# Optimization experiments

Measured on AMD Instinct MI355X. Metric: run time of the kernel, lower is better.

Reference implementation:

```python
import jax, jax.numpy as jnp
import numpy as np

HIDDEN = 4096
W = 16          # wave_units
LN_EPS = 1e-5   # torch LayerNorm default


def _layernorm(x, gamma, beta):
    mu = jnp.mean(x, axis=-1, keepdims=True)
    var = jnp.mean(jnp.square(x - mu), axis=-1, keepdims=True)
    return (x - mu) * jax.lax.rsqrt(var + LN_EPS) * gamma + beta


def setup_inputs() -> dict:
    key = jax.random.key(0)
    ks = jax.random.split(key, 12)
    B, S, H = 4, 4096, HIDDEN
    hidden_states = jax.random.normal(ks[0], (B, S, H), dtype=jnp.float32)
    frequencies = jax.random.uniform(ks[1], (W,), dtype=jnp.float32) * 2.0
    phases = jax.random.uniform(ks[2], (W,), dtype=jnp.float32) * (2 * np.pi)
    coupling_raw = jax.random.normal(ks[3], (W, W), dtype=jnp.float32) * 0.1
    mask = jax.random.uniform(ks[4], (W, W)) < 0.75  # coupling_density
    coupling = coupling_raw * mask.astype(jnp.float32)
    damping = jnp.ones((W,), dtype=jnp.float32) * 0.1
    # input_proj: Linear(H, 2W) -> LN -> SiLU -> Linear(2W, W)
    w1 = jax.random.normal(ks[5], (H, 2 * W), dtype=jnp.float32) * 0.02
    b1 = jnp.zeros((2 * W,), dtype=jnp.float32)
    g1 = jnp.ones((2 * W,), dtype=jnp.float32)
    beta1 = jnp.zeros((2 * W,), dtype=jnp.float32)
    w2 = jax.random.normal(ks[6], (2 * W, W), dtype=jnp.float32) * 0.02
    b2 = jnp.zeros((W,), dtype=jnp.float32)
    # output_proj: Linear(W, 2W) -> LN -> SiLU -> Linear(2W, H)
    w3 = jax.random.normal(ks[7], (W, 2 * W), dtype=jnp.float32) * 0.02
    b3 = jnp.zeros((2 * W,), dtype=jnp.float32)
    g2 = jnp.ones((2 * W,), dtype=jnp.float32)
    beta2 = jnp.zeros((2 * W,), dtype=jnp.float32)
    w4 = jax.random.normal(ks[8], (2 * W, H), dtype=jnp.float32) * 0.02
    b4 = jnp.zeros((H,), dtype=jnp.float32)
    time_step = jnp.float32(0.0)  # buffer; incremented by 0.1 each call
    return dict(hidden_states=hidden_states, frequencies=frequencies, phases=phases,
                coupling=coupling, damping=damping,
                w1=w1, b1=b1, g1=g1, beta1=beta1, w2=w2, b2=b2,
                w3=w3, b3=b3, g2=g2, beta2=beta2, w4=w4, b4=b4,
                time_step=time_step)


def reference(hidden_states, frequencies, phases, coupling, damping,
              w1, b1, g1, beta1, w2, b2,
              w3, b3, g2, beta2, w4, b4, time_step):
    x = hidden_states.astype(jnp.float32)  # [B,S,H]
    t = time_step + 0.1
    # input_proj: [B,S,H] -> [B,S,W]
    h = jnp.einsum('bsh,hd->bsd', x, w1) + b1
    h = jax.nn.silu(_layernorm(h, g1, beta1))
    wave_input = jnp.einsum('bsd,dw->bsw', h, w2) + b2
    # base waves are identical for every (b, s): compute once on [W]
    base_waves = jnp.sin(2 * np.pi * frequencies * t + phases) * jnp.exp(-damping * t)
    coupled = jnp.tanh(base_waves @ coupling)  # [W]
    modulated = coupled * (1.0 + wave_input)   # [B,S,W]
    mean_waves = jnp.mean(modulated, axis=(0, 1))  # [W]
    # buffers start at zero: resonance = 0.9*0 + 0.1*|mean_waves|
    resonance = 0.1 * jnp.abs(mean_waves)
    resonance_factor = jax.nn.sigmoid(jnp.mean(resonance))
    # output_proj: [B,S,W] -> [B,S,H]
    o = jnp.einsum('bsw,wd->bsd', modulated, w3) + b3
    o = jax.nn.silu(_layernorm(o, g2, beta2))
    wave_output = jnp.einsum('bsd,dh->bsh', o, w4) + b4
    return hidden_states + wave_output * resonance_factor
```

## Files before the change

kernel.cpp:

```cpp
#include <hip/hip_runtime.h>
#include <hip/hip_bf16.h>
#include <math.h>

#define HID 4096
#define R_TOTAL 16384

typedef __attribute__((ext_vector_type(8))) short short8;
typedef __attribute__((ext_vector_type(8))) unsigned short ushort8;
typedef __attribute__((ext_vector_type(4))) float f32x4;

__device__ __forceinline__ ushort bfc(float f) {
  __hip_bfloat16 h = __float2bfloat16(f);
  return *(ushort*)&h;
}

__global__ __launch_bounds__(256) void wn_prep(
    const float* __restrict__ w1, const float* __restrict__ w4,
    ushort* __restrict__ w1T, ushort* __restrict__ w4T,
    const float* __restrict__ freq, const float* __restrict__ phases,
    const float* __restrict__ coupling, const float* __restrict__ damping,
    const float* __restrict__ tstep, float* __restrict__ cpl)
{
  __shared__ ushort tile[64*72];
  __shared__ float base[16];
  const int b = blockIdx.x, t = threadIdx.x;
  if (b < 64) {
    #pragma unroll
    for (int i = 0; i < 8; ++i) {
      const int e = t + i*256, kk = e >> 5, c = e & 31;
      tile[c*72 + kk] = bfc(w1[(size_t)(b*64+kk)*32 + c]);
    }
    __syncthreads();
    const int c = t >> 3, j = t & 7;
    ushort8 v;
    #pragma unroll
    for (int q = 0; q < 8; ++q) v[q] = tile[c*72 + j*8 + q];
    *(ushort8*)&w1T[(size_t)c*HID + b*64 + j*8] = v;
  } else if (b < 128) {
    const int b2 = b - 64;
    #pragma unroll
    for (int i = 0; i < 8; ++i) {
      const int e = t + i*256, d = e >> 6, hh = e & 63;
      tile[hh*40 + d] = bfc(w4[(size_t)d*HID + b2*64 + hh]);
    }
    __syncthreads();
    const int hh = t >> 2, j = t & 3;
    ushort8 v;
    #pragma unroll
    for (int q = 0; q < 8; ++q) v[q] = tile[hh*40 + j*8 + q];
    *(ushort8*)&w4T[(size_t)(b2*64+hh)*32 + j*8] = v;
  } else {
    const float tt = tstep[0] + 0.1f;
    if (t < 16)
      base[t] = sinf(6.283185307179586f*freq[t]*tt + phases[t]) * expf(-damping[t]*tt);
    __syncthreads();
    if (t < 16) {
      float s = 0.f;
      #pragma unroll
      for (int i = 0; i < 16; ++i) s += base[i]*coupling[i*16+t];
      cpl[t] = tanhf(s);
    }
  }
}

__global__ __launch_bounds__(256) void wn_phase1(
    const float* __restrict__ x, const ushort* __restrict__ w1T,
    const float* __restrict__ b1, const float* __restrict__ g1,
    const float* __restrict__ beta1, const float* __restrict__ w2,
    const float* __restrict__ b2, const float* __restrict__ w3,
    const float* __restrict__ b3, const float* __restrict__ g2,
    const float* __restrict__ beta2, const float* __restrict__ cpl,
    ushort* __restrict__ o_ws, float* __restrict__ gacc)
{
  __shared__ __align__(16) float lds[10816];
  float* xbuf = lds;
  float* red  = lds;
  float* yl   = lds + 8192;
  float* w2l  = lds + 9248;
  float* w3l  = lds + 9760;
  float* msum = lds + 10272;
  const int t  = threadIdx.x;
  const int r0 = blockIdx.x * 32;

  if (t < 128) *(float4*)&w2l[t*4] = *(const float4*)&w2[t*4];
  else { const int u2 = t-128; *(float4*)&w3l[u2*4] = *(const float4*)&w3[u2*4]; }

  const int w    = t >> 6;
  const int l    = t & 63;
  const int mt   = w & 1, kh = w >> 1;
  const int lrow = l & 15, lkb = l >> 4;
  const int arow = mt*16 + lrow;
  const int aswz = arow & 7;

  f32x4 acc0 = {0.f,0.f,0.f,0.f}, acc1 = {0.f,0.f,0.f,0.f};
  float4 rg0, rg1, rg2, rg3;
  const int e0 = t, e1 = t+256, e2 = t+512, e3 = t+768;
  const int sr0 = e0>>5, su0 = e0&31, sr1 = e1>>5, su1 = e1&31;
  const int sr2 = e2>>5, su2 = e2&31, sr3 = e3>>5, su3 = e3&31;
  const int so0 = sr0*128 + (su0 ^ (sr0&7))*4;
  const int so1 = sr1*128 + (su1 ^ (sr1&7))*4;
  const int so2 = sr2*128 + (su2 ^ (sr2&7))*4;
  const int so3 = sr3*128 + (su3 ^ (sr3&7))*4;

  rg0 = *(const float4*)&x[(size_t)(r0+sr0)*HID + su0*4];
  rg1 = *(const float4*)&x[(size_t)(r0+sr1)*HID + su1*4];
  rg2 = *(const float4*)&x[(size_t)(r0+sr2)*HID + su2*4];
  rg3 = *(const float4*)&x[(size_t)(r0+sr3)*HID + su3*4];
  *(float4*)&xbuf[so0] = rg0;
  *(float4*)&xbuf[so1] = rg1;
  *(float4*)&xbuf[so2] = rg2;
  *(float4*)&xbuf[so3] = rg3;

  for (int it = 0; it < 32; ++it) {
    const int cur = it & 1;
    if (it < 31) {
      const int kc = (it+1)*128;
      rg0 = *(const float4*)&x[(size_t)(r0+sr0)*HID + kc + su0*4];
      rg1 = *(const float4*)&x[(size_t)(r0+sr1)*HID + kc + su1*4];
      rg2 = *(const float4*)&x[(size_t)(r0+sr2)*HID + kc + su2*4];
      rg3 = *(const float4*)&x[(size_t)(r0+sr3)*HID + kc + su3*4];
    }
    __syncthreads();
    const float* xb = &xbuf[cur*4096];
    #pragma unroll
    for (int s = 0; s < 2; ++s) {
      const int k0 = kh*64 + s*32;
      const int ub = (k0 >> 2) + lkb*2;
      const float4 a0 = *(const float4*)&xb[arow*128 + ((ub   ^ aswz))*4];
      const float4 a1 = *(const float4*)&xb[arow*128 + (((ub+1) ^ aswz))*4];
      short8 av;
      av[0] = (short)bfc(a0.x); av[1] = (short)bfc(a0.y);
      av[2] = (short)bfc(a0.z); av[3] = (short)bfc(a0.w);
      av[4] = (short)bfc(a1.x); av[5] = (short)bfc(a1.y);
      av[6] = (short)bfc(a1.z); av[7] = (short)bfc(a1.w);
      const int kg = it*128 + k0 + lkb*8;
      const short8 bv0 = *(const short8*)&w1T[(size_t)lrow*HID + kg];
      const short8 bv1 = *(const short8*)&w1T[(size_t)(16+lrow)*HID + kg];
      acc0 = __builtin_amdgcn_mfma_f32_16x16x32_bf16(av, bv0, acc0, 0, 0, 0);
      acc1 = __builtin_amdgcn_mfma_f32_16x16x32_bf16(av, bv1, acc1, 0, 0, 0);
    }
    __syncthreads();
    if (it < 31) {
      float* xn = &xbuf[(cur^1)*4096];
      *(float4*)&xn[so0] = rg0;
      *(float4*)&xn[so1] = rg1;
      *(float4*)&xn[so2] = rg2;
      *(float4*)&xn[so3] = rg3;
    }
  }
  __syncthreads();
  #pragma unroll
  for (int j = 0; j < 4; ++j) {
    red[kh*1056 + (mt*16 + lkb*4 + j)*33 + lrow]      = acc0[j];
    red[kh*1056 + (mt*16 + lkb*4 + j)*33 + 16 + lrow] = acc1[j];
  }
  __syncthreads();
  #pragma unroll
  for (int i = 0; i < 4; ++i) {
    const int e = t + i*256, row = e >> 5, col = e & 31;
    yl[row*33+col] = red[row*33+col] + red[1056 + row*33+col];
  }
  __syncthreads();
  if (t < 128) {
    const int row = t >> 2, q = t & 3, d0 = q*8;
    float v[8]; float mu = 0.f;
    #pragma unroll
    for (int dd = 0; dd < 8; ++dd) { v[dd] = yl[row*33 + d0+dd] + b1[d0+dd]; mu += v[dd]; }
    mu += __shfl_xor(mu,1); mu += __shfl_xor(mu,2); mu *= (1.f/32.f);
    float var = 0.f;
    #pragma unroll
    for (int dd = 0; dd < 8; ++dd) { const float c = v[dd]-mu; var += c*c; }
    var += __shfl_xor(var,1); var += __shfl_xor(var,2);
    const float rs = rsqrtf(var*(1.f/32.f) + 1e-5f);
    float wiv[16];
    #pragma unroll
    for (int ww = 0; ww < 16; ++ww) wiv[ww] = 0.f;
    #pragma unroll
    for (int dd = 0; dd < 8; ++dd) {
      const float hn = (v[dd]-mu)*rs*g1[d0+dd] + beta1[d0+dd];
      const float sl = hn / (1.f + __expf(-hn));
      const float* wr = &w2l[(d0+dd)*16];
      #pragma unroll
      for (int ww = 0; ww < 16; ++ww) wiv[ww] = fmaf(sl, wr[ww], wiv[ww]);
    }
    #pragma unroll
    for (int ww = 0; ww < 16; ++ww) {
      wiv[ww] += __shfl_xor(wiv[ww],1);
      wiv[ww] += __shfl_xor(wiv[ww],2);
    }
    float mod[16];
    #pragma unroll
    for (int ww = 0; ww < 16; ++ww) mod[ww] = cpl[ww]*(1.f + wiv[ww] + b2[ww]);
    #pragma unroll
    for (int j = 0; j < 4; ++j) msum[row*17 + q*4+j] = mod[q*4+j];
    float p[8];
    #pragma unroll
    for (int dd = 0; dd < 8; ++dd) p[dd] = b3[d0+dd];
    #pragma unroll
    for (int ww = 0; ww < 16; ++ww) {
      const float m = mod[ww];
      const float* wr = &w3l[ww*32 + d0];
      #pragma unroll
      for (int dd = 0; dd < 8; ++dd) p[dd] = fmaf(m, wr[dd], p[dd]);
    }
    float mu2 = 0.f;
    #pragma unroll
    for (int dd = 0; dd < 8; ++dd) mu2 += p[dd];
    mu2 += __shfl_xor(mu2,1); mu2 += __shfl_xor(mu2,2); mu2 *= (1.f/32.f);
    float var2 = 0.f;
    #pragma unroll
    for (int dd = 0; dd < 8; ++dd) { const float c = p[dd]-mu2; var2 += c*c; }
    var2 += __shfl_xor(var2,1); var2 += __shfl_xor(var2,2);
    const float rs2 = rsqrtf(var2*(1.f/32.f) + 1e-5f);
    ushort8 ov;
    #pragma unroll
    for (int dd = 0; dd < 8; ++dd) {
      const float hn = (p[dd]-mu2)*rs2*g2[d0+dd] + beta2[d0+dd];
      ov[dd] = bfc(hn / (1.f + __expf(-hn)));
    }
    *(ushort8*)&o_ws[(size_t)(r0+row)*32 + d0] = ov;
  }
  __syncthreads();
  if (t < 16) {
    float s = 0.f;
    for (int r = 0; r < 32; ++r) s += msum[r*17 + t];
    atomicAdd(gacc + t, s);
  }
}

__global__ void wn_phase2(const float* __restrict__ gacc, float* __restrict__ cpl)
{
  __shared__ float res[16];
  const int t = threadIdx.x;
  if (t < 16) res[t] = 0.1f * fabsf(gacc[t] * (1.f/(float)R_TOTAL));
  __syncthreads();
  if (t == 0) {
    float s = 0.f;
    #pragma unroll
    for (int ww = 0; ww < 16; ++ww) s += res[ww];
    cpl[16] = 1.f / (1.f + expf(-s*(1.f/16.f)));
  }
}

__global__ __launch_bounds__(256) void wn_phase3(
    const float* __restrict__ x, const ushort* __restrict__ o_bf,
    const ushort* __restrict__ w4T, const float* __restrict__ b4,
    const float* __restrict__ cpl, float* __restrict__ out)
{
  const int t = threadIdx.x, l = t & 63, w = t >> 6;
  const int bid = blockIdx.x;
  const int strip = bid & 7, m0 = (bid >> 3) * 64 + w*16;
  const float rf = cpl[16];
  const int lm = l & 15, lkb = l >> 4;
  const short8 bv = *(const short8*)&o_bf[(size_t)(m0+lm)*32 + lkb*8];
  const int mrow = m0 + lm;
  const size_t rowbase = (size_t)mrow*HID + strip*512 + lkb*4;
  #pragma unroll 2
  for (int nt = 0; nt < 32; ++nt) {
    const int n0 = strip*512 + nt*16;
    const short8 av = *(const short8*)&w4T[(size_t)(n0+lm)*32 + lkb*8];
    f32x4 c = {0.f,0.f,0.f,0.f};
    c = __builtin_amdgcn_mfma_f32_16x16x32_bf16(av, bv, c, 0, 0, 0);
    const size_t off = rowbase + (size_t)nt*16;
    const float4 xv  = *(const float4*)&x[off];
    const float4 b4v = *(const float4*)&b4[n0 + lkb*4];
    float4 o2;
    o2.x = fmaf(rf, c[0] + b4v.x, xv.x);
    o2.y = fmaf(rf, c[1] + b4v.y, xv.y);
    o2.z = fmaf(rf, c[2] + b4v.z, xv.z);
    o2.w = fmaf(rf, c[3] + b4v.w, xv.w);
    *(float4*)&out[off] = o2;
  }
}

extern "C" void kernel_launch(void* const* d_in, const int* in_sizes, int n_in,
                              void* d_out, int out_size, void* d_ws, size_t ws_size,
                              hipStream_t stream) {
  const float* x        = (const float*)d_in[0];
  const float* freq     = (const float*)d_in[1];
  const float* phases   = (const float*)d_in[2];
  const float* coupling = (const float*)d_in[3];
  const float* damping  = (const float*)d_in[4];
  const float* w1       = (const float*)d_in[5];
  const float* b1       = (const float*)d_in[6];
  const float* g1       = (const float*)d_in[7];
  const float* beta1    = (const float*)d_in[8];
  const float* w2       = (const float*)d_in[9];
  const float* b2       = (const float*)d_in[10];
  const float* w3       = (const float*)d_in[11];
  const float* b3       = (const float*)d_in[12];
  const float* g2       = (const float*)d_in[13];
  const float* beta2    = (const float*)d_in[14];
  const float* w4       = (const float*)d_in[15];
  const float* b4       = (const float*)d_in[16];
  const float* tstep    = (const float*)d_in[17];
  float* out = (float*)d_out;

  char* wsb = (char*)d_ws;
  ushort* o_bf = (ushort*)wsb;
  ushort* w1T  = (ushort*)(wsb + (1<<20));
  ushort* w4T  = (ushort*)(wsb + (1<<20) + (256<<10));
  float*  gacc = (float*)(wsb + (1<<20) + (512<<10));
  float*  cpl  = gacc + 16;

  hipMemsetAsync(gacc, 0, 16*sizeof(float), stream);
  hipLaunchKernelGGL(wn_prep, dim3(129), dim3(256), 0, stream,
                     w1, w4, w1T, w4T, freq, phases, coupling, damping, tstep, cpl);
  hipLaunchKernelGGL(wn_phase1, dim3(512), dim3(256), 0, stream,
                     x, w1T, b1, g1, beta1, w2, b2, w3, b3, g2, beta2, cpl, o_bf, gacc);
  hipLaunchKernelGGL(wn_phase2, dim3(1), dim3(64), 0, stream, gacc, cpl);
  hipLaunchKernelGGL(wn_phase3, dim3(2048), dim3(256), 0, stream,
                     x, o_bf, w4T, b4, cpl, out);
}
```

Measured before the change: 204.7 us.

## Load x directly into MFMA registers in phase1, split K across eight waves

```diff
diff --git a/kernel.cpp b/kernel.cpp
--- a/kernel.cpp
+++ b/kernel.cpp
@@ -63,7 +63,7 @@
   }
 }
 
-__global__ __launch_bounds__(256) void wn_phase1(
+__global__ __launch_bounds__(512, 4) void wn_phase1(
     const float* __restrict__ x, const ushort* __restrict__ w1T,
     const float* __restrict__ b1, const float* __restrict__ g1,
     const float* __restrict__ beta1, const float* __restrict__ w2,
@@ -72,100 +72,77 @@
     const float* __restrict__ beta2, const float* __restrict__ cpl,
     ushort* __restrict__ o_ws, float* __restrict__ gacc)
 {
-  __shared__ __align__(16) float lds[10816];
-  float* xbuf = lds;
+  __shared__ __align__(16) float lds[6720];
   float* red  = lds;
-  float* yl   = lds + 8192;
-  float* w2l  = lds + 9248;
-  float* w3l  = lds + 9760;
-  float* msum = lds + 10272;
+  float* yl   = lds + 4096;
+  float* w2l  = lds + 5152;
+  float* w3l  = lds + 5664;
+  float* msum = lds + 6176;
   const int t  = threadIdx.x;
   const int r0 = blockIdx.x * 32;
 
   if (t < 128) *(float4*)&w2l[t*4] = *(const float4*)&w2[t*4];
-  else { const int u2 = t-128; *(float4*)&w3l[u2*4] = *(const float4*)&w3[u2*4]; }
-
-  const int w    = t >> 6;
-  const int l    = t & 63;
-  const int mt   = w & 1, kh = w >> 1;
-  const int lrow = l & 15, lkb = l >> 4;
-  const int arow = mt*16 + lrow;
-  const int aswz = arow & 7;
+  else if (t < 256) { const int u2 = t-128; *(float4*)&w3l[u2*4] = *(const float4*)&w3[u2*4]; }
+
+  const int w  = t >> 6, l = t & 63;
+  const int mt = w & 1, kh = w >> 1;
+  const int lr = l & 15, lk = l >> 4;
+  const int row = r0 + mt*16 + lr;
+  const size_t xbase = (size_t)row*HID + kh*1024 + lk*8;
+  const ushort* bp0 = &w1T[(size_t)lr*HID + kh*1024 + lk*8];
+  const ushort* bp1 = bp0 + 16*HID;
 
   f32x4 acc0 = {0.f,0.f,0.f,0.f}, acc1 = {0.f,0.f,0.f,0.f};
-  float4 rg0, rg1, rg2, rg3;
-  const int e0 = t, e1 = t+256, e2 = t+512, e3 = t+768;
-  const int sr0 = e0>>5, su0 = e0&31, sr1 = e1>>5, su1 = e1&31;
-  const int sr2 = e2>>5, su2 = e2&31, sr3 = e3>>5, su3 = e3&31;
-  const int so0 = sr0*128 + (su0 ^ (sr0&7))*4;
-  const int so1 = sr1*128 + (su1 ^ (sr1&7))*4;
-  const int so2 = sr2*128 + (su2 ^ (sr2&7))*4;
-  const int so3 = sr3*128 + (su3 ^ (sr3&7))*4;
-
-  rg0 = *(const float4*)&x[(size_t)(r0+sr0)*HID + su0*4];
-  rg1 = *(const float4*)&x[(size_t)(r0+sr1)*HID + su1*4];
-  rg2 = *(const float4*)&x[(size_t)(r0+sr2)*HID + su2*4];
-  rg3 = *(const float4*)&x[(size_t)(r0+sr3)*HID + su3*4];
-  *(float4*)&xbuf[so0] = rg0;
-  *(float4*)&xbuf[so1] = rg1;
-  *(float4*)&xbuf[so2] = rg2;
-  *(float4*)&xbuf[so3] = rg3;
+  float4 a0 = *(const float4*)&x[xbase];
+  float4 a1 = *(const float4*)&x[xbase + 4];
+  short8 b0 = *(const short8*)bp0;
+  short8 b1v = *(const short8*)bp1;
 
   for (int it = 0; it < 32; ++it) {
-    const int cur = it & 1;
+    float4 na0, na1; short8 nb0, nb1;
     if (it < 31) {
-      const int kc = (it+1)*128;
-      rg0 = *(const float4*)&x[(size_t)(r0+sr0)*HID + kc + su0*4];
-      rg1 = *(const float4*)&x[(size_t)(r0+sr1)*HID + kc + su1*4];
-      rg2 = *(const float4*)&x[(size_t)(r0+sr2)*HID + kc + su2*4];
-      rg3 = *(const float4*)&x[(size_t)(r0+sr3)*HID + kc + su3*4];
-    }
-    __syncthreads();
-    const float* xb = &xbuf[cur*4096];
-    #pragma unroll
-    for (int s = 0; s < 2; ++s) {
-      const int k0 = kh*64 + s*32;
-      const int ub = (k0 >> 2) + lkb*2;
-      const float4 a0 = *(const float4*)&xb[arow*128 + ((ub   ^ aswz))*4];
-      const float4 a1 = *(const float4*)&xb[arow*128 + (((ub+1) ^ aswz))*4];
-      short8 av;
-      av[0] = (short)bfc(a0.x); av[1] = (short)bfc(a0.y);
-      av[2] = (short)bfc(a0.z); av[3] = (short)bfc(a0.w);
-      av[4] = (short)bfc(a1.x); av[5] = (short)bfc(a1.y);
-      av[6] = (short)bfc(a1.z); av[7] = (short)bfc(a1.w);
-      const int kg = it*128 + k0 + lkb*8;
-      const short8 bv0 = *(const short8*)&w1T[(size_t)lrow*HID + kg];
-      const short8 bv1 = *(const short8*)&w1T[(size_t)(16+lrow)*HID + kg];
-      acc0 = __builtin_amdgcn_mfma_f32_16x16x32_bf16(av, bv0, acc0, 0, 0, 0);
-      acc1 = __builtin_amdgcn_mfma_f32_16x16x32_bf16(av, bv1, acc1, 0, 0, 0);
-    }
-    __syncthreads();
-    if (it < 31) {
-      float* xn = &xbuf[(cur^1)*4096];
-      *(float4*)&xn[so0] = rg0;
-      *(float4*)&xn[so1] = rg1;
-      *(float4*)&xn[so2] = rg2;
-      *(float4*)&xn[so3] = rg3;
-    }
-  }
-  __syncthreads();
-  #pragma unroll
-  for (int j = 0; j < 4; ++j) {
-    red[kh*1056 + (mt*16 + lkb*4 + j)*33 + lrow]      = acc0[j];
-    red[kh*1056 + (mt*16 + lkb*4 + j)*33 + 16 + lrow] = acc1[j];
-  }
-  __syncthreads();
-  #pragma unroll
-  for (int i = 0; i < 4; ++i) {
-    const int e = t + i*256, row = e >> 5, col = e & 31;
-    yl[row*33+col] = red[row*33+col] + red[1056 + row*33+col];
+      const int ko = (it+1)*32;
+      na0 = *(const float4*)&x[xbase + ko];
+      na1 = *(const float4*)&x[xbase + ko + 4];
+      nb0 = *(const short8*)(bp0 + ko);
+      nb1 = *(const short8*)(bp1 + ko);
+    }
+    short8 av;
+    av[0] = (short)bfc(a0.x); av[1] = (short)bfc(a0.y);
+    av[2] = (short)bfc(a0.z); av[3] = (short)bfc(a0.w);
+    av[4] = (short)bfc(a1.x); av[5] = (short)bfc(a1.y);
+    av[6] = (short)bfc(a1.z); av[7] = (short)bfc(a1.w);
+    acc0 = __builtin_amdgcn_mfma_f32_16x16x32_bf16(av, b0, acc0, 0, 0, 0);
+    acc1 = __builtin_amdgcn_mfma_f32_16x16x32_bf16(av, b1v, acc1, 0, 0, 0);
+    a0 = na0; a1 = na1; b0 = nb0; b1v = nb1;
+  }
+  {
+    float* rp = &red[w*512 + l];
+    #pragma unroll
+    for (int j = 0; j < 4; ++j) { rp[j*64] = acc0[j]; rp[(4+j)*64] = acc1[j]; }
   }
   __syncthreads();
   if (t < 128) {
-    const int row = t >> 2, q = t & 3, d0 = q*8;
+    const int m2 = t >> 6, l2 = t & 63;
+    const int rr = m2*16 + (l2 >> 4)*4, cc = l2 & 15;
+    #pragma unroll
+    for (int j = 0; j < 4; ++j) {
+      float s0 = 0.f, s1 = 0.f;
+      #pragma unroll
+      for (int k = 0; k < 4; ++k) {
+        s0 += red[(m2 + 2*k)*512 + j*64 + l2];
+        s1 += red[(m2 + 2*k)*512 + (4+j)*64 + l2];
+      }
+      yl[(rr+j)*33 + cc]      = s0;
+      yl[(rr+j)*33 + 16 + cc] = s1;
+    }
+  }
+  __syncthreads();
+  if (t < 128) {
+    const int row2 = t >> 2, q = t & 3, d0 = q*8;
     float v[8]; float mu = 0.f;
     #pragma unroll
-    for (int dd = 0; dd < 8; ++dd) { v[dd] = yl[row*33 + d0+dd] + b1[d0+dd]; mu += v[dd]; }
+    for (int dd = 0; dd < 8; ++dd) { v[dd] = yl[row2*33 + d0+dd] + b1[d0+dd]; mu += v[dd]; }
     mu += __shfl_xor(mu,1); mu += __shfl_xor(mu,2); mu *= (1.f/32.f);
     float var = 0.f;
     #pragma unroll
@@ -192,7 +169,7 @@
     #pragma unroll
     for (int ww = 0; ww < 16; ++ww) mod[ww] = cpl[ww]*(1.f + wiv[ww] + b2[ww]);
     #pragma unroll
-    for (int j = 0; j < 4; ++j) msum[row*17 + q*4+j] = mod[q*4+j];
+    for (int j = 0; j < 4; ++j) msum[row2*17 + q*4+j] = mod[q*4+j];
     float p[8];
     #pragma unroll
     for (int dd = 0; dd < 8; ++dd) p[dd] = b3[d0+dd];
@@ -218,7 +195,7 @@
       const float hn = (p[dd]-mu2)*rs2*g2[d0+dd] + beta2[d0+dd];
       ov[dd] = bfc(hn / (1.f + __expf(-hn)));
     }
-    *(ushort8*)&o_ws[(size_t)(r0+row)*32 + d0] = ov;
+    *(ushort8*)&o_ws[(size_t)(r0+row2)*32 + d0] = ov;
   }
   __syncthreads();
   if (t < 16) {
@@ -255,7 +232,7 @@
   const short8 bv = *(const short8*)&o_bf[(size_t)(m0+lm)*32 + lkb*8];
   const int mrow = m0 + lm;
   const size_t rowbase = (size_t)mrow*HID + strip*512 + lkb*4;
-  #pragma unroll 2
+  #pragma unroll 4
   for (int nt = 0; nt < 32; ++nt) {
     const int n0 = strip*512 + nt*16;
     const short8 av = *(const short8*)&w4T[(size_t)(n0+lm)*32 + lkb*8];
@@ -306,7 +283,7 @@
   hipMemsetAsync(gacc, 0, 16*sizeof(float), stream);
   hipLaunchKernelGGL(wn_prep, dim3(129), dim3(256), 0, stream,
                      w1, w4, w1T, w4T, freq, phases, coupling, damping, tstep, cpl);
-  hipLaunchKernelGGL(wn_phase1, dim3(512), dim3(256), 0, stream,
+  hipLaunchKernelGGL(wn_phase1, dim3(512), dim3(512), 0, stream,
                      x, w1T, b1, g1, beta1, w2, b2, w3, b3, g2, beta2, cpl, o_bf, gacc);
   hipLaunchKernelGGL(wn_phase2, dim3(1), dim3(64), 0, stream, gacc, cpl);
   hipLaunchKernelGGL(wn_phase3, dim3(2048), dim3(256), 0, stream,
```

New measurement: 255.4 us. 24.7% more time.

## Stage x tile as bf16 in LDS, reverse phase3 row order, nontemporal output stores

Applied to the files above, without the earlier changes.

```diff
diff --git a/kernel.cpp b/kernel.cpp
--- a/kernel.cpp
+++ b/kernel.cpp
@@ -72,80 +72,85 @@
     const float* __restrict__ beta2, const float* __restrict__ cpl,
     ushort* __restrict__ o_ws, float* __restrict__ gacc)
 {
-  __shared__ __align__(16) float lds[10816];
-  float* xbuf = lds;
+  __shared__ __align__(16) float lds[6720];
+  ushort* xb  = (ushort*)lds;
   float* red  = lds;
-  float* yl   = lds + 8192;
-  float* w2l  = lds + 9248;
-  float* w3l  = lds + 9760;
-  float* msum = lds + 10272;
+  float* yl   = lds + 4096;
+  float* w2l  = lds + 5152;
+  float* w3l  = lds + 5664;
+  float* msum = lds + 6176;
   const int t  = threadIdx.x;
   const int r0 = blockIdx.x * 32;
 
   if (t < 128) *(float4*)&w2l[t*4] = *(const float4*)&w2[t*4];
   else { const int u2 = t-128; *(float4*)&w3l[u2*4] = *(const float4*)&w3[u2*4]; }
 
-  const int w    = t >> 6;
-  const int l    = t & 63;
+  const int srow = t >> 3, sc = t & 7;
+  const int wg0   = ((sc*2) ^ ((srow&7)<<1));
+  const int wbase = srow*128 + wg0*8;
+  const float* xp = &x[(size_t)(r0+srow)*HID + sc*16];
+
+  const int w    = t >> 6, l = t & 63;
   const int mt   = w & 1, kh = w >> 1;
   const int lrow = l & 15, lkb = l >> 4;
   const int arow = mt*16 + lrow;
-  const int aswz = arow & 7;
+  const int rsw  = (arow&7) << 1;
+  const int ra_s0 = arow*128 + ((kh*8 +     lkb) ^ rsw)*8;
+  const int ra_s1 = arow*128 + ((kh*8 + 4 + lkb) ^ rsw)*8;
+  const ushort* bp0 = &w1T[(size_t)lrow*HID + kh*64 + lkb*8];
+  const ushort* bp1 = bp0 + 16*HID;
 
   f32x4 acc0 = {0.f,0.f,0.f,0.f}, acc1 = {0.f,0.f,0.f,0.f};
   float4 rg0, rg1, rg2, rg3;
-  const int e0 = t, e1 = t+256, e2 = t+512, e3 = t+768;
-  const int sr0 = e0>>5, su0 = e0&31, sr1 = e1>>5, su1 = e1&31;
-  const int sr2 = e2>>5, su2 = e2&31, sr3 = e3>>5, su3 = e3&31;
-  const int so0 = sr0*128 + (su0 ^ (sr0&7))*4;
-  const int so1 = sr1*128 + (su1 ^ (sr1&7))*4;
-  const int so2 = sr2*128 + (su2 ^ (sr2&7))*4;
-  const int so3 = sr3*128 + (su3 ^ (sr3&7))*4;
-
-  rg0 = *(const float4*)&x[(size_t)(r0+sr0)*HID + su0*4];
-  rg1 = *(const float4*)&x[(size_t)(r0+sr1)*HID + su1*4];
-  rg2 = *(const float4*)&x[(size_t)(r0+sr2)*HID + su2*4];
-  rg3 = *(const float4*)&x[(size_t)(r0+sr3)*HID + su3*4];
-  *(float4*)&xbuf[so0] = rg0;
-  *(float4*)&xbuf[so1] = rg1;
-  *(float4*)&xbuf[so2] = rg2;
-  *(float4*)&xbuf[so3] = rg3;
+
+  rg0 = *(const float4*)&xp[0];
+  rg1 = *(const float4*)&xp[4];
+  rg2 = *(const float4*)&xp[8];
+  rg3 = *(const float4*)&xp[12];
+  {
+    ushort8 v0, v1;
+    v0[0]=bfc(rg0.x); v0[1]=bfc(rg0.y); v0[2]=bfc(rg0.z); v0[3]=bfc(rg0.w);
+    v0[4]=bfc(rg1.x); v0[5]=bfc(rg1.y); v0[6]=bfc(rg1.z); v0[7]=bfc(rg1.w);
+    v1[0]=bfc(rg2.x); v1[1]=bfc(rg2.y); v1[2]=bfc(rg2.z); v1[3]=bfc(rg2.w);
+    v1[4]=bfc(rg3.x); v1[5]=bfc(rg3.y); v1[6]=bfc(rg3.z); v1[7]=bfc(rg3.w);
+    *(ushort8*)&xb[wbase]     = v0;
+    *(ushort8*)&xb[wbase + 8] = v1;
+  }
 
   for (int it = 0; it < 32; ++it) {
     const int cur = it & 1;
     if (it < 31) {
       const int kc = (it+1)*128;
-      rg0 = *(const float4*)&x[(size_t)(r0+sr0)*HID + kc + su0*4];
-      rg1 = *(const float4*)&x[(size_t)(r0+sr1)*HID + kc + su1*4];
-      rg2 = *(const float4*)&x[(size_t)(r0+sr2)*HID + kc + su2*4];
-      rg3 = *(const float4*)&x[(size_t)(r0+sr3)*HID + kc + su3*4];
-    }
-    __syncthreads();
-    const float* xb = &xbuf[cur*4096];
-    #pragma unroll
-    for (int s = 0; s < 2; ++s) {
-      const int k0 = kh*64 + s*32;
-      const int ub = (k0 >> 2) + lkb*2;
-      const float4 a0 = *(const float4*)&xb[arow*128 + ((ub   ^ aswz))*4];
-      const float4 a1 = *(const float4*)&xb[arow*128 + (((ub+1) ^ aswz))*4];
-      short8 av;
-      av[0] = (short)bfc(a0.x); av[1] = (short)bfc(a0.y);
-      av[2] = (short)bfc(a0.z); av[3] = (short)bfc(a0.w);
-      av[4] = (short)bfc(a1.x); av[5] = (short)bfc(a1.y);
-      av[6] = (short)bfc(a1.z); av[7] = (short)bfc(a1.w);
-      const int kg = it*128 + k0 + lkb*8;
-      const short8 bv0 = *(const short8*)&w1T[(size_t)lrow*HID + kg];
-      const short8 bv1 = *(const short8*)&w1T[(size_t)(16+lrow)*HID + kg];
-      acc0 = __builtin_amdgcn_mfma_f32_16x16x32_bf16(av, bv0, acc0, 0, 0, 0);
-      acc1 = __builtin_amdgcn_mfma_f32_16x16x32_bf16(av, bv1, acc1, 0, 0, 0);
+      rg0 = *(const float4*)&xp[kc];
+      rg1 = *(const float4*)&xp[kc + 4];
+      rg2 = *(const float4*)&xp[kc + 8];
+      rg3 = *(const float4*)&xp[kc + 12];
+    }
+    __syncthreads();
+    {
+      const ushort* xc = &xb[cur*4096];
+      const int kg = it*128;
+      const short8 av0 = *(const short8*)&xc[ra_s0];
+      const short8 bv00 = *(const short8*)(bp0 + kg);
+      const short8 bv01 = *(const short8*)(bp1 + kg);
+      acc0 = __builtin_amdgcn_mfma_f32_16x16x32_bf16(av0, bv00, acc0, 0, 0, 0);
+      acc1 = __builtin_amdgcn_mfma_f32_16x16x32_bf16(av0, bv01, acc1, 0, 0, 0);
+      const short8 av1 = *(const short8*)&xc[ra_s1];
+      const short8 bv10 = *(const short8*)(bp0 + kg + 32);
+      const short8 bv11 = *(const short8*)(bp1 + kg + 32);
+      acc0 = __builtin_amdgcn_mfma_f32_16x16x32_bf16(av1, bv10, acc0, 0, 0, 0);
+      acc1 = __builtin_amdgcn_mfma_f32_16x16x32_bf16(av1, bv11, acc1, 0, 0, 0);
     }
     __syncthreads();
     if (it < 31) {
-      float* xn = &xbuf[(cur^1)*4096];
-      *(float4*)&xn[so0] = rg0;
-      *(float4*)&xn[so1] = rg1;
-      *(float4*)&xn[so2] = rg2;
-      *(float4*)&xn[so3] = rg3;
+      ushort* xn = &xb[(cur^1)*4096];
+      ushort8 v0, v1;
+      v0[0]=bfc(rg0.x); v0[1]=bfc(rg0.y); v0[2]=bfc(rg0.z); v0[3]=bfc(rg0.w);
+      v0[4]=bfc(rg1.x); v0[5]=bfc(rg1.y); v0[6]=bfc(rg1.z); v0[7]=bfc(rg1.w);
+      v1[0]=bfc(rg2.x); v1[1]=bfc(rg2.y); v1[2]=bfc(rg2.z); v1[3]=bfc(rg2.w);
+      v1[4]=bfc(rg3.x); v1[5]=bfc(rg3.y); v1[6]=bfc(rg3.z); v1[7]=bfc(rg3.w);
+      *(ushort8*)&xn[wbase]     = v0;
+      *(ushort8*)&xn[wbase + 8] = v1;
     }
   }
   __syncthreads();
@@ -249,7 +254,8 @@
 {
   const int t = threadIdx.x, l = t & 63, w = t >> 6;
   const int bid = blockIdx.x;
-  const int strip = bid & 7, m0 = (bid >> 3) * 64 + w*16;
+  const int strip = bid & 7;
+  const int m0 = (255 - (bid >> 3)) * 64 + w*16;
   const float rf = cpl[16];
   const int lm = l & 15, lkb = l >> 4;
   const short8 bv = *(const short8*)&o_bf[(size_t)(m0+lm)*32 + lkb*8];
@@ -264,12 +270,12 @@
     const size_t off = rowbase + (size_t)nt*16;
     const float4 xv  = *(const float4*)&x[off];
     const float4 b4v = *(const float4*)&b4[n0 + lkb*4];
-    float4 o2;
-    o2.x = fmaf(rf, c[0] + b4v.x, xv.x);
-    o2.y = fmaf(rf, c[1] + b4v.y, xv.y);
-    o2.z = fmaf(rf, c[2] + b4v.z, xv.z);
-    o2.w = fmaf(rf, c[3] + b4v.w, xv.w);
-    *(float4*)&out[off] = o2;
+    f32x4 o2;
+    o2[0] = fmaf(rf, c[0] + b4v.x, xv.x);
+    o2[1] = fmaf(rf, c[1] + b4v.y, xv.y);
+    o2[2] = fmaf(rf, c[2] + b4v.z, xv.z);
+    o2[3] = fmaf(rf, c[3] + b4v.w, xv.w);
+    __builtin_nontemporal_store(o2, (f32x4*)&out[off]);
   }
 }
 
```

New measurement: 187.1 us. 8.6% less time.
